# Kernel optimization log

Measured on AMD Instinct MI355X. Metric: run time of the kernel, lower is better.

## Reference

```python
import jax, jax.numpy as jnp
import numpy as np

B, T, D = 4, 4096, 1024
NUM_HEADS = 8
HEAD_DIM = D // NUM_HEADS
MLP_HIDDEN = int(2.0 * D)
EPS = 1e-6


def fake_quantize_int8(w):
    # per-row int8 fake quant with straight-through estimator
    scale = jnp.max(jnp.abs(w), axis=1, keepdims=True) / 127.0
    scale = jnp.maximum(scale, 1e-8)
    w_q = jnp.round(w / scale) * scale
    return w + jax.lax.stop_gradient(w_q - w)


def rmsnorm(x, w, eps=EPS):
    xf = x.astype(jnp.float32)
    y = xf * jax.lax.rsqrt(jnp.mean(xf * xf, axis=-1, keepdims=True) + eps)
    return y.astype(x.dtype) * w


def setup_inputs() -> dict:
    key = jax.random.key(0)
    k = jax.random.split(key, 5)
    x = jax.random.normal(k[0], (B, T, D), jnp.float32)
    in_proj_w = 0.02 * jax.random.normal(k[1], (2 * D, D), jnp.float32)
    o_proj_w = 0.02 * jax.random.normal(k[2], (D, D), jnp.float32)
    mlp_in_w = 0.02 * jax.random.normal(k[3], (MLP_HIDDEN, D), jnp.float32)
    mlp_out_w = 0.02 * jax.random.normal(k[4], (D, MLP_HIDDEN), jnp.float32)
    # decay filter: exp(-0.1*t) repeated over heads -> [seq_len, num_heads]
    fixed_filter = jnp.exp(-0.1 * jnp.arange(T, dtype=jnp.float32))[:, None] * jnp.ones((1, NUM_HEADS), jnp.float32)
    norm1_w = jnp.ones((D,), jnp.float32)
    norm2_w = jnp.ones((D,), jnp.float32)
    return {"x": x, "norm1_w": norm1_w, "norm2_w": norm2_w, "in_proj_w": in_proj_w,
            "o_proj_w": o_proj_w, "mlp_in_w": mlp_in_w, "mlp_out_w": mlp_out_w,
            "fixed_filter": fixed_filter}


def reference(x, norm1_w, norm2_w, in_proj_w, o_proj_w, mlp_in_w, mlp_out_w, fixed_filter):
    Bx, Tx, C = x.shape
    residual = x
    h = rmsnorm(x, norm1_w)
    qkv = h @ fake_quantize_int8(in_proj_w).T          # [B,T,2C]
    signal, gate = qkv[..., :C], qkv[..., C:]
    # [B, H, T, Dh] in fp32
    s = signal.reshape(Bx, Tx, NUM_HEADS, HEAD_DIM).transpose(0, 2, 1, 3).astype(jnp.float32)
    filt = fixed_filter[:Tx].T[None, :, :, None].astype(jnp.float32)  # [1,H,T,1]
    n = 2 * Tx  # zero-pad to 2T for linear (causal) convolution
    S_fft = jnp.fft.rfft(s, n=n, axis=2)
    H_fft = jnp.fft.rfft(filt, n=n, axis=2)
    y = jnp.fft.irfft(S_fft * H_fft, n=n, axis=2)[:, :, :Tx, :]
    y = y.transpose(0, 2, 1, 3).reshape(Bx, Tx, C).astype(x.dtype)
    out = y * jax.nn.silu(gate)
    x2 = residual + out @ fake_quantize_int8(o_proj_w).T
    residual2 = x2
    h2 = rmsnorm(x2, norm2_w)
    m = jax.nn.gelu(h2 @ fake_quantize_int8(mlp_in_w).T, approximate=False)
    return residual2 + m @ fake_quantize_int8(mlp_out_w).T
```

## Files before the change

kernel.cpp:

```cpp
#include <hip/hip_runtime.h>

typedef unsigned short u16;
typedef __attribute__((ext_vector_type(8))) short s16x8;
typedef __attribute__((ext_vector_type(4))) float f32x4;

#define BM 128
#define BN 128
#define BK 32

__device__ __forceinline__ float bf2f(u16 u) {
    union { unsigned int u; float f; } v; v.u = ((unsigned int)u) << 16; return v.f;
}
__device__ __forceinline__ u16 f2bf(float f) {
    union { float f; unsigned int u; } v; v.f = f;
    unsigned int r = v.u + 0x7FFFu + ((v.u >> 16) & 1u);
    return (u16)(r >> 16);
}

__device__ __forceinline__ void async16(const u16* g, u16* l) {
    __builtin_amdgcn_global_load_lds(
        (const __attribute__((address_space(1))) void*)g,
        (__attribute__((address_space(3))) void*)l,
        16, 0, 0);
}

__global__ __launch_bounds__(256) void detect_dtype(const u16* __restrict__ x,
                                                    int* __restrict__ flag) {
    const int t = threadIdx.x;
    float mx = 0.f;
    #pragma unroll
    for (int j = 0; j < 16; ++j) mx = fmaxf(mx, fabsf(bf2f(x[t * 16 + j])));
    #pragma unroll
    for (int off = 32; off; off >>= 1) mx = fmaxf(mx, __shfl_down(mx, off));
    __shared__ float red[4];
    const int lane = t & 63, wave = t >> 6;
    if (lane == 0) red[wave] = mx;
    __syncthreads();
    if (t == 0) {
        float m = fmaxf(fmaxf(red[0], red[1]), fmaxf(red[2], red[3]));
        *flag = (m > 1e4f) ? 1 : 0;
    }
}

__device__ __forceinline__ float load_raw(const void* p, size_t i, int f32) {
    return f32 ? ((const float*)p)[i] : bf2f(((const u16*)p)[i]);
}

__global__ __launch_bounds__(256) void quant_rows(const void* __restrict__ w,
                                                  u16* __restrict__ wq, int L,
                                                  const int* __restrict__ flagp) {
    const int f32 = *flagp;
    const int row = blockIdx.x;
    const int t = threadIdx.x;
    const size_t base = (size_t)row * L;
    float mx = 0.f;
    for (int i = t; i < L; i += 256) mx = fmaxf(mx, fabsf(load_raw(w, base + i, f32)));
    #pragma unroll
    for (int off = 32; off; off >>= 1) mx = fmaxf(mx, __shfl_down(mx, off));
    __shared__ float red[4];
    __shared__ float s_scale;
    const int lane = t & 63, wave = t >> 6;
    if (lane == 0) red[wave] = mx;
    __syncthreads();
    if (t == 0) {
        float m = fmaxf(fmaxf(red[0], red[1]), fmaxf(red[2], red[3]));
        s_scale = fmaxf(m / 127.f, 1e-8f);
    }
    __syncthreads();
    const float scale = s_scale;
    for (int i = t; i < L; i += 256) {
        float v = load_raw(w, base + i, f32);
        wq[base + i] = f2bf(rintf(v / scale) * scale);
    }
}

template <int IN_RAW>
__global__ __launch_bounds__(256) void rmsnorm_k(const void* __restrict__ x,
                                                 const void* __restrict__ w,
                                                 u16* __restrict__ out,
                                                 const int* __restrict__ flagp) {
    const int f32 = *flagp;
    const int row = blockIdx.x;
    const int t = threadIdx.x;
    float x0, x1, x2, x3;
    if (IN_RAW && f32) {
        float4 xv = ((const float4*)x)[(size_t)row * 256 + t];
        x0 = xv.x; x1 = xv.y; x2 = xv.z; x3 = xv.w;
    } else {
        ushort4 xv = *(const ushort4*)((const u16*)x + (size_t)row * 1024 + t * 4);
        x0 = bf2f(xv.x); x1 = bf2f(xv.y); x2 = bf2f(xv.z); x3 = bf2f(xv.w);
    }
    float s = x0 * x0 + x1 * x1 + x2 * x2 + x3 * x3;
    #pragma unroll
    for (int off = 32; off; off >>= 1) s += __shfl_down(s, off);
    __shared__ float red[4];
    __shared__ float s_rs;
    const int lane = t & 63, wave = t >> 6;
    if (lane == 0) red[wave] = s;
    __syncthreads();
    if (t == 0) {
        float tot = red[0] + red[1] + red[2] + red[3];
        s_rs = 1.0f / sqrtf(tot * (1.0f / 1024.0f) + 1e-6f);
    }
    __syncthreads();
    const float rs = s_rs;
    float w0, w1, w2, w3;
    if (f32) {
        float4 wv = ((const float4*)w)[t];
        w0 = wv.x; w1 = wv.y; w2 = wv.z; w3 = wv.w;
    } else {
        ushort4 wv = *(const ushort4*)((const u16*)w + t * 4);
        w0 = bf2f(wv.x); w1 = bf2f(wv.y); w2 = bf2f(wv.z); w3 = bf2f(wv.w);
    }
    ushort4 o;
    o.x = f2bf(bf2f(f2bf(x0 * rs)) * w0);
    o.y = f2bf(bf2f(f2bf(x1 * rs)) * w1);
    o.z = f2bf(bf2f(f2bf(x2 * rs)) * w2);
    o.w = f2bf(bf2f(f2bf(x3 * rs)) * w3);
    *(ushort4*)(out + (size_t)row * 1024 + t * 4) = o;
}

__global__ __launch_bounds__(256) void scan_silu(u16* __restrict__ qkv) {
    const int c = blockIdx.x * 256 + threadIdx.x;
    const int chunk = blockIdx.y;
    const int b = blockIdx.z;
    const int t0 = chunk * 256;
    const int ts = (t0 >= 256) ? (t0 - 256) : 0;
    const float r = 0.90483741803595957f;
    const size_t base = (size_t)b * 4096 * 2048 + c;
    float y = 0.f;
    for (int tt = ts; tt < t0; ++tt) {
        y = y * r + bf2f(qkv[base + (size_t)tt * 2048]);
    }
    for (int tt = t0; tt < t0 + 256; ++tt) {
        const size_t idx = base + (size_t)tt * 2048;
        y = y * r + bf2f(qkv[idx]);
        float g = bf2f(qkv[idx + 1024]);
        float sg = g / (1.f + expf(-g));
        qkv[idx + 1024] = f2bf(y * sg);
    }
}

template <int EPI>
__global__ __launch_bounds__(256) void gemm_bt(const u16* __restrict__ A, int lda,
                                               const u16* __restrict__ B,
                                               const void* __restrict__ RES, int res_raw,
                                               void* __restrict__ C, int c_raw,
                                               int M, int N, int K,
                                               const int* __restrict__ flagp) {
    const int f32 = *flagp;
    __shared__ u16 As[BM * BK];
    __shared__ u16 Bs[BN * BK];
    const int t = threadIdx.x;
    const int lane = t & 63, wave = t >> 6;
    const int wm = wave >> 1, wn = wave & 1;
    const int lr = lane & 15, quad = lane >> 4;
    const int m0 = blockIdx.y * BM, n0 = blockIdx.x * BN;

    const int srow = wave * 16 + (lane >> 2);
    const int scol = (lane & 3) * 8;
    const u16* Ag0 = A + (size_t)(m0 + srow) * lda + scol;
    const u16* Ag1 = A + (size_t)(m0 + srow + 64) * lda + scol;
    const u16* Bg0 = B + (size_t)(n0 + srow) * K + scol;
    const u16* Bg1 = B + (size_t)(n0 + srow + 64) * K + scol;
    u16* Al0 = &As[(wave * 16) * BK];
    u16* Al1 = &As[(64 + wave * 16) * BK];
    u16* Bl0 = &Bs[(wave * 16) * BK];
    u16* Bl1 = &Bs[(64 + wave * 16) * BK];

    f32x4 acc[4][4];
    #pragma unroll
    for (int i = 0; i < 4; ++i)
        #pragma unroll
        for (int j = 0; j < 4; ++j) acc[i][j] = (f32x4){0.f, 0.f, 0.f, 0.f};

    for (int k0 = 0; k0 < K; k0 += BK) {
        __syncthreads();
        async16(Ag0 + k0, Al0);
        async16(Ag1 + k0, Al1);
        async16(Bg0 + k0, Bl0);
        async16(Bg1 + k0, Bl1);
        __syncthreads();
        s16x8 af[4], bfr[4];
        #pragma unroll
        for (int i = 0; i < 4; ++i)
            af[i] = *(const s16x8*)&As[(wm * 64 + i * 16 + lr) * BK + quad * 8];
        #pragma unroll
        for (int j = 0; j < 4; ++j)
            bfr[j] = *(const s16x8*)&Bs[(wn * 64 + j * 16 + lr) * BK + quad * 8];
        #pragma unroll
        for (int i = 0; i < 4; ++i)
            #pragma unroll
            for (int j = 0; j < 4; ++j)
                acc[i][j] = __builtin_amdgcn_mfma_f32_16x16x32_bf16(
                    af[i], bfr[j], acc[i][j], 0, 0, 0);
    }

    #pragma unroll
    for (int i = 0; i < 4; ++i) {
        #pragma unroll
        for (int j = 0; j < 4; ++j) {
            #pragma unroll
            for (int r = 0; r < 4; ++r) {
                int gm = m0 + wm * 64 + i * 16 + quad * 4 + r;
                int gn = n0 + wn * 64 + j * 16 + lr;
                size_t idx = (size_t)gm * N + gn;
                float v = acc[i][j][r];
                if (EPI == 1) {
                    float rv = (res_raw && f32) ? ((const float*)RES)[idx]
                                                : bf2f(((const u16*)RES)[idx]);
                    v += rv;
                }
                if (EPI == 2) v = 0.5f * v * (1.0f + erff(v * 0.70710678118654752f));
                if (c_raw && f32) ((float*)C)[idx] = v;
                else              ((u16*)C)[idx] = f2bf(v);
            }
        }
    }
}

extern "C" void kernel_launch(void* const* d_in, const int* in_sizes, int n_in,
                              void* d_out, int out_size, void* d_ws, size_t ws_size,
                              hipStream_t stream) {
    const void* x    = d_in[0];
    const void* n1w  = d_in[1];
    const void* n2w  = d_in[2];
    const void* w_in = d_in[3];
    const void* w_o  = d_in[4];
    const void* w_mi = d_in[5];
    const void* w_mo = d_in[6];

    char* ws = (char*)d_ws;
    int* flag  = (int*)(ws + 0);
    u16* wq_in = (u16*)(ws + 256);
    u16* wq_o  = (u16*)(ws + 256 + 4194304);
    u16* wq_mi = (u16*)(ws + 256 + 6291456);
    u16* wq_mo = (u16*)(ws + 256 + 10485760);
    u16* hbuf  = (u16*)(ws + 256 + 14680064);
    u16* qkv   = (u16*)(ws + 256 + 48234496);
    u16* x2b   = (u16*)(ws + 256 + 115343360);

    detect_dtype<<<1, 256, 0, stream>>>((const u16*)x, flag);

    quant_rows<<<2048, 256, 0, stream>>>(w_in, wq_in, 1024, flag);
    quant_rows<<<1024, 256, 0, stream>>>(w_o,  wq_o,  1024, flag);
    quant_rows<<<2048, 256, 0, stream>>>(w_mi, wq_mi, 1024, flag);
    quant_rows<<<1024, 256, 0, stream>>>(w_mo, wq_mo, 2048, flag);

    rmsnorm_k<1><<<16384, 256, 0, stream>>>(x, n1w, hbuf, flag);
    gemm_bt<0><<<dim3(16, 128), 256, 0, stream>>>(hbuf, 1024, wq_in,
                                                  nullptr, 0, qkv, 0,
                                                  16384, 2048, 1024, flag);
    scan_silu<<<dim3(4, 16, 4), 256, 0, stream>>>(qkv);
    gemm_bt<1><<<dim3(8, 128), 256, 0, stream>>>(qkv + 1024, 2048, wq_o,
                                                 x, 1, x2b, 0,
                                                 16384, 1024, 1024, flag);
    rmsnorm_k<0><<<16384, 256, 0, stream>>>(x2b, n2w, hbuf, flag);
    gemm_bt<2><<<dim3(16, 128), 256, 0, stream>>>(hbuf, 1024, wq_mi,
                                                  nullptr, 0, qkv, 0,
                                                  16384, 2048, 1024, flag);
    gemm_bt<1><<<dim3(8, 128), 256, 0, stream>>>(qkv, 2048, wq_mo,
                                                 x2b, 0, d_out, 1,
                                                 16384, 1024, 2048, flag);
}
```

Measured before the change: 732.8 us.

## Double GEMM K-step to 64 and remap blocks for XCD-aware L2 locality

The GEMM now loads two 32-wide K slices per iteration into separate LDS buffers. This halves the number of barrier pairs and gives more MFMA work per sync. The grid becomes 1D, with a block-index remap that sends all N tiles of a given M row-block to the same XCD (d&7), so A tiles are reused within that XCD's L2. LDS use doubles, which may reduce occupancy, and the remap assumes the M tile count is divisible by 8.

New measurement: 673.7 us. -8.1%, faster.

```diff
diff --git a/kernel.cpp b/kernel.cpp
--- a/kernel.cpp
+++ b/kernel.cpp
@@ -6,7 +6,6 @@
 
 #define BM 128
 #define BN 128
-#define BK 32
 
 __device__ __forceinline__ float bf2f(u16 u) {
     union { unsigned int u; float f; } v; v.u = ((unsigned int)u) << 16; return v.f;
@@ -149,13 +148,19 @@
                                                int M, int N, int K,
                                                const int* __restrict__ flagp) {
     const int f32 = *flagp;
-    __shared__ u16 As[BM * BK];
-    __shared__ u16 Bs[BN * BK];
+    __shared__ u16 As0[BM * 32], As1[BM * 32];
+    __shared__ u16 Bs0[BN * 32], Bs1[BN * 32];
     const int t = threadIdx.x;
     const int lane = t & 63, wave = t >> 6;
     const int wm = wave >> 1, wn = wave & 1;
     const int lr = lane & 15, quad = lane >> 4;
-    const int m0 = blockIdx.y * BM, n0 = blockIdx.x * BN;
+
+    const int NT = N >> 7;
+    const int d = blockIdx.x;
+    const int xcd = d & 7;
+    const int s = d >> 3;
+    const int m0 = ((s / NT) * 8 + xcd) * BM;
+    const int n0 = (s % NT) * BN;
 
     const int srow = wave * 16 + (lane >> 2);
     const int scol = (lane & 3) * 8;
@@ -163,10 +168,14 @@
     const u16* Ag1 = A + (size_t)(m0 + srow + 64) * lda + scol;
     const u16* Bg0 = B + (size_t)(n0 + srow) * K + scol;
     const u16* Bg1 = B + (size_t)(n0 + srow + 64) * K + scol;
-    u16* Al0 = &As[(wave * 16) * BK];
-    u16* Al1 = &As[(64 + wave * 16) * BK];
-    u16* Bl0 = &Bs[(wave * 16) * BK];
-    u16* Bl1 = &Bs[(64 + wave * 16) * BK];
+    u16* Al0a = &As0[(wave * 16) * 32];
+    u16* Al1a = &As0[(64 + wave * 16) * 32];
+    u16* Bl0a = &Bs0[(wave * 16) * 32];
+    u16* Bl1a = &Bs0[(64 + wave * 16) * 32];
+    u16* Al0b = &As1[(wave * 16) * 32];
+    u16* Al1b = &As1[(64 + wave * 16) * 32];
+    u16* Bl0b = &Bs1[(wave * 16) * 32];
+    u16* Bl1b = &Bs1[(64 + wave * 16) * 32];
 
     f32x4 acc[4][4];
     #pragma unroll
@@ -174,26 +183,35 @@
         #pragma unroll
         for (int j = 0; j < 4; ++j) acc[i][j] = (f32x4){0.f, 0.f, 0.f, 0.f};
 
-    for (int k0 = 0; k0 < K; k0 += BK) {
+    for (int k0 = 0; k0 < K; k0 += 64) {
         __syncthreads();
-        async16(Ag0 + k0, Al0);
-        async16(Ag1 + k0, Al1);
-        async16(Bg0 + k0, Bl0);
-        async16(Bg1 + k0, Bl1);
+        async16(Ag0 + k0, Al0a);
+        async16(Ag1 + k0, Al1a);
+        async16(Bg0 + k0, Bl0a);
+        async16(Bg1 + k0, Bl1a);
+        async16(Ag0 + k0 + 32, Al0b);
+        async16(Ag1 + k0 + 32, Al1b);
+        async16(Bg0 + k0 + 32, Bl0b);
+        async16(Bg1 + k0 + 32, Bl1b);
         __syncthreads();
-        s16x8 af[4], bfr[4];
         #pragma unroll
-        for (int i = 0; i < 4; ++i)
-            af[i] = *(const s16x8*)&As[(wm * 64 + i * 16 + lr) * BK + quad * 8];
-        #pragma unroll
-        for (int j = 0; j < 4; ++j)
-            bfr[j] = *(const s16x8*)&Bs[(wn * 64 + j * 16 + lr) * BK + quad * 8];
-        #pragma unroll
-        for (int i = 0; i < 4; ++i)
+        for (int sl = 0; sl < 2; ++sl) {
+            const u16* Asl = sl ? As1 : As0;
+            const u16* Bsl = sl ? Bs1 : Bs0;
+            s16x8 af[4], bfr[4];
+            #pragma unroll
+            for (int i = 0; i < 4; ++i)
+                af[i] = *(const s16x8*)&Asl[(wm * 64 + i * 16 + lr) * 32 + quad * 8];
             #pragma unroll
             for (int j = 0; j < 4; ++j)
-                acc[i][j] = __builtin_amdgcn_mfma_f32_16x16x32_bf16(
-                    af[i], bfr[j], acc[i][j], 0, 0, 0);
+                bfr[j] = *(const s16x8*)&Bsl[(wn * 64 + j * 16 + lr) * 32 + quad * 8];
+            #pragma unroll
+            for (int i = 0; i < 4; ++i)
+                #pragma unroll
+                for (int j = 0; j < 4; ++j)
+                    acc[i][j] = __builtin_amdgcn_mfma_f32_16x16x32_bf16(
+                        af[i], bfr[j], acc[i][j], 0, 0, 0);
+        }
     }
 
     #pragma unroll
@@ -248,18 +266,18 @@
     quant_rows<<<1024, 256, 0, stream>>>(w_mo, wq_mo, 2048, flag);
 
     rmsnorm_k<1><<<16384, 256, 0, stream>>>(x, n1w, hbuf, flag);
-    gemm_bt<0><<<dim3(16, 128), 256, 0, stream>>>(hbuf, 1024, wq_in,
-                                                  nullptr, 0, qkv, 0,
-                                                  16384, 2048, 1024, flag);
+    gemm_bt<0><<<2048, 256, 0, stream>>>(hbuf, 1024, wq_in,
+                                         nullptr, 0, qkv, 0,
+                                         16384, 2048, 1024, flag);
     scan_silu<<<dim3(4, 16, 4), 256, 0, stream>>>(qkv);
-    gemm_bt<1><<<dim3(8, 128), 256, 0, stream>>>(qkv + 1024, 2048, wq_o,
-                                                 x, 1, x2b, 0,
-                                                 16384, 1024, 1024, flag);
+    gemm_bt<1><<<1024, 256, 0, stream>>>(qkv + 1024, 2048, wq_o,
+                                         x, 1, x2b, 0,
+                                         16384, 1024, 1024, flag);
     rmsnorm_k<0><<<16384, 256, 0, stream>>>(x2b, n2w, hbuf, flag);
-    gemm_bt<2><<<dim3(16, 128), 256, 0, stream>>>(hbuf, 1024, wq_mi,
-                                                  nullptr, 0, qkv, 0,
-                                                  16384, 2048, 1024, flag);
-    gemm_bt<1><<<dim3(8, 128), 256, 0, stream>>>(qkv, 2048, wq_mo,
-                                                 x2b, 0, d_out, 1,
-                                                 16384, 1024, 2048, flag);
-}
+    gemm_bt<2><<<2048, 256, 0, stream>>>(hbuf, 1024, wq_mi,
+                                         nullptr, 0, qkv, 0,
+                                         16384, 2048, 1024, flag);
+    gemm_bt<1><<<1024, 256, 0, stream>>>(qkv, 2048, wq_mo,
+                                         x2b, 0, d_out, 1,
+                                         16384, 1024, 2048, flag);
+}
```
